# Performance work log

Hardware: AMD Instinct MI355X
Metric: run time of the kernel (lower is better)

The kernel has to match this reference:

```python
import jax, jax.numpy as jnp
import numpy as np

B, L, D = 16, 1024, 256
H, FF = 8, 2048
DH = D // H
EPS = 1e-5


def setup_inputs() -> dict:
    key = jax.random.key(0)
    ks = jax.random.split(key, 13)
    s = 0.02
    return {
        "x": jax.random.normal(ks[0], (B, L, D), jnp.float32),
        "Wq": jax.random.normal(ks[1], (D, D), jnp.float32) * s,
        "bq": jnp.zeros((D,), jnp.float32),
        "Wk": jax.random.normal(ks[2], (D, D), jnp.float32) * s,
        "bk": jnp.zeros((D,), jnp.float32),
        "Wv": jax.random.normal(ks[3], (D, D), jnp.float32) * s,
        "bv": jnp.zeros((D,), jnp.float32),
        "Wo": jax.random.normal(ks[4], (D, D), jnp.float32) * s,
        "bo": jnp.zeros((D,), jnp.float32),
        "W1": jax.random.normal(ks[5], (D, FF), jnp.float32) * s,
        "b1": jnp.zeros((FF,), jnp.float32),
        "W2": jax.random.normal(ks[6], (FF, D), jnp.float32) * s,
        "b2": jnp.zeros((D,), jnp.float32),
        "g1": jnp.ones((D,), jnp.float32),
        "be1": jnp.zeros((D,), jnp.float32),
        "g2": jnp.ones((D,), jnp.float32),
        "be2": jnp.zeros((D,), jnp.float32),
    }


def _layernorm(x, g, b):
    m = jnp.mean(x, axis=-1, keepdims=True)
    v = jnp.mean(jnp.square(x - m), axis=-1, keepdims=True)
    return (x - m) * jax.lax.rsqrt(v + EPS) * g + b


def reference(x, Wq, bq, Wk, bk, Wv, bv, Wo, bo, W1, b1, W2, b2, g1, be1, g2, be2):
    b, l, d = x.shape
    # QKV projections, split heads (torch split/cat == reshape to [b,l,H,dh])
    q = (x @ Wq + bq).reshape(b, l, H, DH)
    k = (x @ Wk + bk).reshape(b, l, H, DH)
    v = (x @ Wv + bv).reshape(b, l, H, DH)
    # scaled dot-product attention per head
    scores = jnp.einsum("bqhd,bkhd->bhqk", q, k) / np.float32(DH) ** 0.5
    attn = jax.nn.softmax(scores, axis=-1)
    o = jnp.einsum("bhqk,bkhd->bqhd", attn, v).reshape(b, l, d)
    o = o @ Wo + bo
    # residual + LN1 (dropout p=0.0 -> identity)
    h = _layernorm(x + o, g1, be1)
    # FFN + residual + LN2
    ff = jax.nn.relu(h @ W1 + b1) @ W2 + b2
    return _layernorm(h + ff, g2, be2)
```

## Files before the change

kernel.cpp:

```cpp
#include <hip/hip_runtime.h>
#include <math.h>

#define B_  16
#define L_  1024
#define D_  256
#define H_  8
#define DH_ 32
#define FF_ 2048
#define NROW (B_*L_)
#define QKVS 768

typedef __attribute__((ext_vector_type(8))) short short8;
typedef __attribute__((ext_vector_type(4))) short short4v;
typedef __attribute__((ext_vector_type(4))) float f32x4;
typedef __attribute__((ext_vector_type(4))) unsigned uint4v;
typedef unsigned short ushortT;

__device__ inline ushortT f2bf(float f) {
    unsigned u = __builtin_bit_cast(unsigned, f);
    u += 0x7fffu + ((u >> 16) & 1u);
    return (ushortT)(u >> 16);
}

__device__ inline float bf2f(ushortT u) {
    return __builtin_bit_cast(float, (unsigned)u << 16);
}

__device__ inline float fexp2(float x) {
#if __has_builtin(__builtin_amdgcn_exp2f)
    return __builtin_amdgcn_exp2f(x);
#else
    return exp2f(x);
#endif
}

__device__ inline void gload_lds16(const ushortT* g, ushortT* l) {
    __builtin_amdgcn_global_load_lds(
        (const __attribute__((address_space(1))) unsigned*)g,
        (__attribute__((address_space(3))) unsigned*)l, 16, 0, 0);
}

__device__ inline unsigned lds_addr(const void* p) {
    return (unsigned)(size_t)(const __attribute__((address_space(3))) void*)p;
}

template<bool RELU, bool OBF16>
__global__ __launch_bounds__(256)
void gemm_bf16_kernel(const ushortT* __restrict__ A, const ushortT* __restrict__ Bt,
                      const float* __restrict__ bias, void* __restrict__ Cv,
                      int M, int N, int K, int ldb, int ldc)
{
    __shared__ ushortT As[2][128 * 32];
    __shared__ ushortT Bs[2][128 * 32];

    const int tid   = threadIdx.x;
    const int w     = tid >> 6;
    const int lane  = tid & 63;
    const int qlane = lane & 15;
    const int g     = lane >> 4;
    const int wm    = w >> 1, wn = w & 1;
    const int m0    = blockIdx.y * 128;
    const int n0    = blockIdx.x * 128;

    int srowA[2], sq[2];
    #pragma unroll
    for (int j = 0; j < 2; ++j) {
        int idx = (j * 4 + w) * 64 + lane;
        srowA[j] = idx >> 2;
        sq[j]    = idx & 3;
    }

    f32x4 acc[4][4];
    #pragma unroll
    for (int mi = 0; mi < 4; ++mi)
        #pragma unroll
        for (int ni = 0; ni < 4; ++ni)
            acc[mi][ni] = (f32x4){0.f, 0.f, 0.f, 0.f};

    auto stage = [&](int buf, int kt) {
        const int k0 = kt * 32;
        #pragma unroll
        for (int j = 0; j < 2; ++j) {
            gload_lds16(A + (size_t)(m0 + srowA[j]) * K + k0 + sq[j] * 8,
                        &As[buf][(j * 4 + w) * 512]);
            gload_lds16(Bt + (size_t)(n0 + srowA[j]) * ldb + k0 + sq[j] * 8,
                        &Bs[buf][(j * 4 + w) * 512]);
        }
    };

    stage(0, 0);
    __syncthreads();

    const int nt = K >> 5;
    for (int t = 0; t < nt; ++t) {
        const int cur = t & 1;
        if (t + 1 < nt) stage(cur ^ 1, t + 1);

        short8 af[4], bfr[4];
        #pragma unroll
        for (int mi = 0; mi < 4; ++mi)
            af[mi] = *(const short8*)&As[cur][(wm * 64 + mi * 16 + qlane) * 32 + g * 8];
        #pragma unroll
        for (int ni = 0; ni < 4; ++ni)
            bfr[ni] = *(const short8*)&Bs[cur][(wn * 64 + ni * 16 + qlane) * 32 + g * 8];

        #pragma unroll
        for (int mi = 0; mi < 4; ++mi)
            #pragma unroll
            for (int ni = 0; ni < 4; ++ni)
                acc[mi][ni] = __builtin_amdgcn_mfma_f32_16x16x32_bf16(
                    af[mi], bfr[ni], acc[mi][ni], 0, 0, 0);

        __syncthreads();
    }

    #pragma unroll
    for (int mi = 0; mi < 4; ++mi) {
        #pragma unroll
        for (int ni = 0; ni < 4; ++ni) {
            const int n = n0 + wn * 64 + ni * 16 + qlane;
            const float bval = bias ? bias[n] : 0.f;
            #pragma unroll
            for (int r = 0; r < 4; ++r) {
                const int m = m0 + wm * 64 + mi * 16 + 4 * g + r;
                float v = acc[mi][ni][r] + bval;
                if (RELU)  v = fmaxf(v, 0.f);
                if (OBF16) ((ushortT*)Cv)[(size_t)m * ldc + n] = f2bf(v);
                else       ((float*)Cv)[(size_t)m * ldc + n] = v;
            }
        }
    }
}

template<bool RESF32, bool OBF16>
__global__ __launch_bounds__(512)
void gemm_ln_kernel(const ushortT* __restrict__ A, const ushortT* __restrict__ Bt,
                    const float* __restrict__ bias, const void* __restrict__ resid,
                    const float* __restrict__ gamma, const float* __restrict__ beta,
                    void* __restrict__ out, int K)
{
    __shared__ ushortT As[2][64 * 32];
    __shared__ ushortT Bs[2][256 * 32];
    __shared__ float part[8][32][2];
    __shared__ float rstat[64][2];

    const int tid   = threadIdx.x;
    const int w     = tid >> 6;
    const int lane  = tid & 63;
    const int qlane = lane & 15;
    const int g     = lane >> 4;
    const int wm    = w >> 2, wn = w & 3;
    const int m0    = blockIdx.x * 64;

    f32x4 acc[2][4];
    #pragma unroll
    for (int mi = 0; mi < 2; ++mi)
        #pragma unroll
        for (int ni = 0; ni < 4; ++ni)
            acc[mi][ni] = (f32x4){0.f, 0.f, 0.f, 0.f};

    const int r4 = lane >> 2, q8 = (lane & 3) * 8;

    auto stage = [&](int buf, int kt) {
        const int k0 = kt * 32;
        if (w < 4)
            gload_lds16(A + (size_t)(m0 + w * 16 + r4) * K + k0 + q8,
                        &As[buf][w * 512]);
        #pragma unroll
        for (int j = 0; j < 2; ++j) {
            const int c = w * 2 + j;
            gload_lds16(Bt + (size_t)(c * 16 + r4) * K + k0 + q8,
                        &Bs[buf][c * 512]);
        }
    };

    stage(0, 0);
    __syncthreads();

    const int nt = K >> 5;
    for (int t = 0; t < nt; ++t) {
        const int cur = t & 1;
        if (t + 1 < nt) stage(cur ^ 1, t + 1);

        short8 af[2], bfr[4];
        #pragma unroll
        for (int mi = 0; mi < 2; ++mi)
            af[mi] = *(const short8*)&As[cur][(wm * 32 + mi * 16 + qlane) * 32 + g * 8];
        #pragma unroll
        for (int ni = 0; ni < 4; ++ni)
            bfr[ni] = *(const short8*)&Bs[cur][(wn * 64 + ni * 16 + qlane) * 32 + g * 8];

        #pragma unroll
        for (int mi = 0; mi < 2; ++mi)
            #pragma unroll
            for (int ni = 0; ni < 4; ++ni)
                acc[mi][ni] = __builtin_amdgcn_mfma_f32_16x16x32_bf16(
                    af[mi], bfr[ni], acc[mi][ni], 0, 0, 0);

        __syncthreads();
    }

    #pragma unroll
    for (int ni = 0; ni < 4; ++ni) {
        const int n = wn * 64 + ni * 16 + qlane;
        const float bv = bias[n];
        #pragma unroll
        for (int mi = 0; mi < 2; ++mi)
            #pragma unroll
            for (int r = 0; r < 4; ++r) {
                const size_t m = (size_t)(m0 + wm * 32 + mi * 16 + 4 * g + r);
                float rv;
                if (RESF32) rv = ((const float*)resid)[m * 256 + n];
                else        rv = bf2f(((const ushortT*)resid)[m * 256 + n]);
                acc[mi][ni][r] += bv + rv;
            }
    }

    #pragma unroll
    for (int mi = 0; mi < 2; ++mi)
        #pragma unroll
        for (int r = 0; r < 4; ++r) {
            float s = 0.f, sq = 0.f;
            #pragma unroll
            for (int ni = 0; ni < 4; ++ni) {
                float hv = acc[mi][ni][r];
                s += hv; sq += hv * hv;
            }
            #pragma unroll
            for (int off = 1; off < 16; off <<= 1) {
                s  += __shfl_xor(s, off);
                sq += __shfl_xor(sq, off);
            }
            if (qlane == 0) {
                part[w][mi * 16 + 4 * g + r][0] = s;
                part[w][mi * 16 + 4 * g + r][1] = sq;
            }
        }
    __syncthreads();
    if (tid < 64) {
        const int wmr = tid >> 5, lrow = tid & 31;
        float s = 0.f, sq = 0.f;
        #pragma unroll
        for (int j = 0; j < 4; ++j) {
            s  += part[wmr * 4 + j][lrow][0];
            sq += part[wmr * 4 + j][lrow][1];
        }
        const float mean = s * (1.f / 256.f);
        const float var  = sq * (1.f / 256.f) - mean * mean;
        rstat[tid][0] = mean;
        rstat[tid][1] = rsqrtf(var + 1e-5f);
    }
    __syncthreads();

    float gam[4], bet[4];
    #pragma unroll
    for (int ni = 0; ni < 4; ++ni) {
        gam[ni] = gamma[wn * 64 + ni * 16 + qlane];
        bet[ni] = beta [wn * 64 + ni * 16 + qlane];
    }
    #pragma unroll
    for (int mi = 0; mi < 2; ++mi)
        #pragma unroll
        for (int r = 0; r < 4; ++r) {
            const int rloc = wm * 32 + mi * 16 + 4 * g + r;
            const float mean = rstat[rloc][0], rinv = rstat[rloc][1];
            const size_t m = (size_t)(m0 + rloc);
            #pragma unroll
            for (int ni = 0; ni < 4; ++ni) {
                const int n = wn * 64 + ni * 16 + qlane;
                const float val = (acc[mi][ni][r] - mean) * rinv * gam[ni] + bet[ni];
                if (OBF16) ((ushortT*)out)[m * 256 + n] = f2bf(val);
                else       ((float*)out)[m * 256 + n] = val;
            }
        }
}

__global__ __launch_bounds__(256)
void attn_mfma_kernel(const ushortT* __restrict__ qkv, ushortT* __restrict__ o)
{
    __shared__ __align__(16) ushortT K4[2][2048];
    __shared__ __align__(16) ushortT Vs[2][2048];

    const int tid   = threadIdx.x;
    const int lane  = tid & 63;
    const int w     = tid >> 6;
    const int qlane = lane & 15;
    const int g     = lane >> 4;

    const int bid = blockIdx.x;
    const int bh  = bid & 127;
    const int b   = bh >> 3;
    const int h   = bh & 7;
    const int q0  = (bid >> 7) * 64;

    const size_t inbase = (size_t)b * L_ * QKVS + h * 32;
    const size_t obase  = (size_t)b * L_ * 256 + h * 32;

    const short8 qf = *(const short8*)(qkv + inbase + (size_t)(q0 + w * 16 + qlane) * QKVS + g * 8);

    f32x4 ot0 = {0.f, 0.f, 0.f, 0.f}, ot1 = {0.f, 0.f, 0.f, 0.f};
    float l_reg = 0.f;

    const float CEXP = 0.25503540f;

    const int skey = tid >> 2;
    const int sg   = tid & 3;
    const ushortT* ksrc = qkv + inbase + 256 + sg * 8 + (size_t)skey * QKVS;
    const ushortT* vsrc = qkv + inbase + 512 + sg * 8 + (size_t)skey * QKVS;

    char* K4b = (char*)&K4[0][0];
    char* Vsb = (char*)&Vs[0][0];

    const unsigned vwoff = ((unsigned)((skey >> 2) * 2 + (sg >> 1))) * 128u +
                           ((unsigned)(skey & 3)) * 32u +
                           ((((unsigned)(sg & 1)) ^ ((unsigned)(sg >> 1))) * 16u);
    unsigned kwoff = (unsigned)sg * 1024u + (unsigned)skey * 16u;
    kwoff ^= (kwoff >> 5) & 0x60;
    unsigned kroff[4];
    #pragma unroll
    for (int kt4 = 0; kt4 < 4; ++kt4) {
        unsigned off = (unsigned)g * 1024u + (unsigned)(kt4 * 16 + qlane) * 16u;
        kroff[kt4] = off ^ ((off >> 5) & 0x60);
    }
    const unsigned vrbase  = lds_addr(&Vs[0][0]) + 256u * (unsigned)g + 8u * (unsigned)qlane;
    const unsigned vrbase2 = vrbase ^ 64u;

    short8 kreg = *(const short8*)ksrc;
    short8 vreg = *(const short8*)vsrc;

    #pragma unroll 2
    for (int t = 0; t < L_ / 64; ++t) {
        const unsigned bo = (unsigned)(t & 1) * 4096u;
        *(short8*)(K4b + bo + kwoff) = kreg;
        *(short8*)(Vsb + bo + vwoff) = vreg;
        if (t + 1 < L_ / 64) {
            const size_t roff = (size_t)((t + 1) * 64) * QKVS;
            kreg = *(const short8*)(ksrc + roff);
            vreg = *(const short8*)(vsrc + roff);
        }
        __syncthreads();

        f32x4 st[4];
        __builtin_amdgcn_s_setprio(1);
        #pragma unroll
        for (int kt4 = 0; kt4 < 4; ++kt4) {
            short8 kf = *(const short8*)(K4b + bo + kroff[kt4]);
            st[kt4] = __builtin_amdgcn_mfma_f32_16x16x32_bf16(kf, qf, (f32x4){0.f,0.f,0.f,0.f}, 0, 0, 0);
        }
        __builtin_amdgcn_s_setprio(0);

        float p[16];
        float s4[4];
        #pragma unroll
        for (int kt4 = 0; kt4 < 4; ++kt4) {
            #pragma unroll
            for (int r = 0; r < 4; ++r)
                p[kt4 * 4 + r] = fexp2(st[kt4][r] * CEXP);
            s4[kt4] = (p[kt4*4] + p[kt4*4+1]) + (p[kt4*4+2] + p[kt4*4+3]);
        }
        float ssum = (s4[0] + s4[1]) + (s4[2] + s4[3]);
        ssum += __shfl_xor(ssum, 16);
        ssum += __shfl_xor(ssum, 32);
        l_reg += ssum;

        unsigned pk_[8];
        #pragma unroll
        for (int i = 0; i < 8; ++i)
            asm("v_cvt_pk_bf16_f32 %0, %1, %2" : "=v"(pk_[i]) : "v"(p[2*i]), "v"(p[2*i+1]));
        const short8 pa0 = __builtin_bit_cast(short8, (uint4v){pk_[0], pk_[1], pk_[2], pk_[3]});
        const short8 pa1 = __builtin_bit_cast(short8, (uint4v){pk_[4], pk_[5], pk_[6], pk_[7]});

        const unsigned va  = vrbase  + bo;
        const unsigned va2 = vrbase2 + bo;
        __builtin_amdgcn_s_setprio(1);
        {
            short4v v00, v01, v10, v11;
            asm volatile("ds_read_b64_tr_b16 %0, %1"             : "=v"(v00) : "v"(va));
            asm volatile("ds_read_b64_tr_b16 %0, %1 offset:1024" : "=v"(v01) : "v"(va));
            asm volatile("ds_read_b64_tr_b16 %0, %1 offset:128"  : "=v"(v10) : "v"(va2));
            asm volatile("ds_read_b64_tr_b16 %0, %1 offset:1152" : "=v"(v11) : "v"(va2));
            asm volatile("s_waitcnt lgkmcnt(0)" ::: "memory");
            __builtin_amdgcn_sched_barrier(0);
            short8 vb0 = __builtin_shufflevector(v00, v01, 0,1,2,3,4,5,6,7);
            short8 vb1 = __builtin_shufflevector(v10, v11, 0,1,2,3,4,5,6,7);
            ot0 = __builtin_amdgcn_mfma_f32_16x16x32_bf16(pa0, vb0, ot0, 0, 0, 0);
            ot1 = __builtin_amdgcn_mfma_f32_16x16x32_bf16(pa0, vb1, ot1, 0, 0, 0);
        }
        {
            short4v v00, v01, v10, v11;
            asm volatile("ds_read_b64_tr_b16 %0, %1 offset:2048" : "=v"(v00) : "v"(va));
            asm volatile("ds_read_b64_tr_b16 %0, %1 offset:3072" : "=v"(v01) : "v"(va));
            asm volatile("ds_read_b64_tr_b16 %0, %1 offset:2176" : "=v"(v10) : "v"(va2));
            asm volatile("ds_read_b64_tr_b16 %0, %1 offset:3200" : "=v"(v11) : "v"(va2));
            asm volatile("s_waitcnt lgkmcnt(0)" ::: "memory");
            __builtin_amdgcn_sched_barrier(0);
            short8 vb0 = __builtin_shufflevector(v00, v01, 0,1,2,3,4,5,6,7);
            short8 vb1 = __builtin_shufflevector(v10, v11, 0,1,2,3,4,5,6,7);
            ot0 = __builtin_amdgcn_mfma_f32_16x16x32_bf16(pa1, vb0, ot0, 0, 0, 0);
            ot1 = __builtin_amdgcn_mfma_f32_16x16x32_bf16(pa1, vb1, ot1, 0, 0, 0);
        }
        __builtin_amdgcn_s_setprio(0);
    }

    const float linv = 1.f / l_reg;
    #pragma unroll
    for (int r = 0; r < 4; ++r) {
        float lr = __shfl(linv, 4 * g + r);
        size_t row = (size_t)(q0 + w * 16 + 4 * g + r);
        ushortT* op = o + obase + row * 256;
        op[qlane]      = f2bf(ot0[r] * lr);
        op[16 + qlane] = f2bf(ot1[r] * lr);
    }
}

__global__ __launch_bounds__(256)
void prep_kernel(const float* __restrict__ x, ushortT* __restrict__ xb,
                 const float* __restrict__ Wq, const float* __restrict__ Wk,
                 const float* __restrict__ Wv, const float* __restrict__ Wo,
                 ushortT* __restrict__ Wqkvb, ushortT* __restrict__ Wob,
                 const float* __restrict__ W1, ushortT* __restrict__ W1b,
                 const float* __restrict__ W2, ushortT* __restrict__ W2b,
                 const float* __restrict__ bq, const float* __restrict__ bk,
                 const float* __restrict__ bv, float* __restrict__ bqkv)
{
    __shared__ float t[32][33];
    const int bid = blockIdx.x;
    const int tid = threadIdx.x;

    if (bid < 4096) {
        const int i = (bid * 256 + tid) * 4;
        float4 v = *reinterpret_cast<const float4*>(x + i);
        unsigned p0 = (unsigned)f2bf(v.x) | ((unsigned)f2bf(v.y) << 16);
        unsigned p1 = (unsigned)f2bf(v.z) | ((unsigned)f2bf(v.w) << 16);
        uint2 u = {p0, p1};
        *reinterpret_cast<uint2*>(xb + i) = u;
        return;
    }
    int i = bid - 4096;
    const float* W; ushortT* Wt; int K, N, bx, by;
    if (i < 256) {
        const int which = i >> 6, j = i & 63;
        bx = j & 7; by = j >> 3; K = 256; N = 256;
        W  = which == 0 ? Wq : which == 1 ? Wk : which == 2 ? Wv : Wo;
        Wt = which == 0 ? Wqkvb : which == 1 ? Wqkvb + 65536
           : which == 2 ? Wqkvb + 131072 : Wob;
    } else if (i < 768) {
        const int j = i - 256; bx = j & 63; by = j >> 6; K = 256; N = 2048;
        W = W1; Wt = W1b;
    } else if (i < 1280) {
        const int j = i - 768; bx = j & 7; by = j >> 3; K = 2048; N = 256;
        W = W2; Wt = W2b;
    } else {
        for (int k = tid; k < 768; k += 256)
            bqkv[k] = k < 256 ? bq[k] : (k < 512 ? bk[k - 256] : bv[k - 512]);
        return;
    }
    const int tx = tid & 31, ty = tid >> 5;
    const int k0 = by * 32, n0 = bx * 32;
    #pragma unroll
    for (int r = ty; r < 32; r += 8) t[r][tx] = W[(size_t)(k0 + r) * N + n0 + tx];
    __syncthreads();
    #pragma unroll
    for (int r = ty; r < 32; r += 8) Wt[(size_t)(n0 + r) * K + k0 + tx] = f2bf(t[tx][r]);
}

extern "C" void kernel_launch(void* const* d_in, const int* in_sizes, int n_in,
                              void* d_out, int out_size, void* d_ws, size_t ws_size,
                              hipStream_t stream)
{
    const float* x   = (const float*)d_in[0];
    const float* Wq  = (const float*)d_in[1];
    const float* bq  = (const float*)d_in[2];
    const float* Wk  = (const float*)d_in[3];
    const float* bk  = (const float*)d_in[4];
    const float* Wv  = (const float*)d_in[5];
    const float* bv  = (const float*)d_in[6];
    const float* Wo  = (const float*)d_in[7];
    const float* bo  = (const float*)d_in[8];
    const float* W1  = (const float*)d_in[9];
    const float* b1  = (const float*)d_in[10];
    const float* W2  = (const float*)d_in[11];
    const float* b2  = (const float*)d_in[12];
    const float* g1  = (const float*)d_in[13];
    const float* be1 = (const float*)d_in[14];
    const float* g2  = (const float*)d_in[15];
    const float* be2 = (const float*)d_in[16];
    float* out = (float*)d_out;

    char* wsb = (char*)d_ws;
    const size_t MB = (size_t)1 << 20;
    ushortT* Wqkvb = (ushortT*)(wsb);
    ushortT* Wob   = (ushortT*)(wsb + 393216);
    ushortT* W1b   = (ushortT*)(wsb + 1 * MB);
    ushortT* W2b   = (ushortT*)(wsb + 2 * MB);
    float*   bqkv  = (float*)  (wsb + 3 * MB);
    ushortT* xb  = (ushortT*)(wsb + 4 * MB);
    ushortT* qkv = (ushortT*)(wsb + 12 * MB);
    ushortT* ob  = (ushortT*)(wsb + 36 * MB);
    ushortT* hb  = (ushortT*)(wsb + 4 * MB);
    ushortT* f1  = (ushortT*)(wsb + 12 * MB);

    prep_kernel<<<dim3(5377), dim3(256), 0, stream>>>(
        x, xb, Wq, Wk, Wv, Wo, Wqkvb, Wob, W1, W1b, W2, W2b, bq, bk, bv, bqkv);

    gemm_bf16_kernel<false, true><<<dim3(6, 128), dim3(256), 0, stream>>>(
        xb, Wqkvb, bqkv, qkv, NROW, QKVS, 256, 256, QKVS);

    attn_mfma_kernel<<<dim3(2048), dim3(256), 0, stream>>>(qkv, ob);

    gemm_ln_kernel<true, true><<<dim3(256), dim3(512), 0, stream>>>(
        ob, Wob, bo, x, g1, be1, hb, 256);

    gemm_bf16_kernel<true, true><<<dim3(16, 128), dim3(256), 0, stream>>>(
        hb, W1b, b1, f1, NROW, FF_, 256, 256, FF_);

    gemm_ln_kernel<false, false><<<dim3(256), dim3(512), 0, stream>>>(
        f1, W2b, b2, hb, g2, be2, out, 2048);
}
```

Before: 153.8 us.

## Shrink GEMM+LayerNorm row tile to 32 rows and launch 512 blocks

The fused GEMM+LayerNorm kernel now handles 32 rows per block instead of 64. Each of the 8 waves owns a 32-column slice across all rows, and the grid doubles to 512 blocks. The aim is better occupancy across the CUs: 256 blocks is roughly one per CU on MI355X, so doubling the count should fill the device and hide load latency. In exchange, each block reloads the full 256-column B tile for half as many rows, doubling weight traffic per output row and lowering MFMA reuse per LDS load.

```diff
diff --git a/kernel.cpp b/kernel.cpp
--- a/kernel.cpp
+++ b/kernel.cpp
@@ -139,38 +139,35 @@
                     const float* __restrict__ gamma, const float* __restrict__ beta,
                     void* __restrict__ out, int K)
 {
-    __shared__ ushortT As[2][64 * 32];
+    __shared__ ushortT As[2][32 * 32];
     __shared__ ushortT Bs[2][256 * 32];
     __shared__ float part[8][32][2];
-    __shared__ float rstat[64][2];
+    __shared__ float rstat[32][2];
 
     const int tid   = threadIdx.x;
     const int w     = tid >> 6;
     const int lane  = tid & 63;
     const int qlane = lane & 15;
     const int g     = lane >> 4;
-    const int wm    = w >> 2, wn = w & 3;
-    const int m0    = blockIdx.x * 64;
-
-    f32x4 acc[2][4];
+    const int m0    = blockIdx.x * 32;
+
+    f32x4 acc[2][2];
     #pragma unroll
     for (int mi = 0; mi < 2; ++mi)
         #pragma unroll
-        for (int ni = 0; ni < 4; ++ni)
+        for (int ni = 0; ni < 2; ++ni)
             acc[mi][ni] = (f32x4){0.f, 0.f, 0.f, 0.f};
-
-    const int r4 = lane >> 2, q8 = (lane & 3) * 8;
 
     auto stage = [&](int buf, int kt) {
         const int k0 = kt * 32;
-        if (w < 4)
-            gload_lds16(A + (size_t)(m0 + w * 16 + r4) * K + k0 + q8,
-                        &As[buf][w * 512]);
+        if (tid < 128)
+            gload_lds16(A + (size_t)(m0 + (tid >> 2)) * K + k0 + (tid & 3) * 8,
+                        &As[buf][tid * 8]);
         #pragma unroll
         for (int j = 0; j < 2; ++j) {
-            const int c = w * 2 + j;
-            gload_lds16(Bt + (size_t)(c * 16 + r4) * K + k0 + q8,
-                        &Bs[buf][c * 512]);
+            const int idx = j * 512 + tid;
+            gload_lds16(Bt + (size_t)(idx >> 2) * K + k0 + (idx & 3) * 8,
+                        &Bs[buf][idx * 8]);
         }
     };
 
@@ -182,18 +179,18 @@
         const int cur = t & 1;
         if (t + 1 < nt) stage(cur ^ 1, t + 1);
 
-        short8 af[2], bfr[4];
+        short8 af[2], bfr[2];
         #pragma unroll
         for (int mi = 0; mi < 2; ++mi)
-            af[mi] = *(const short8*)&As[cur][(wm * 32 + mi * 16 + qlane) * 32 + g * 8];
-        #pragma unroll
-        for (int ni = 0; ni < 4; ++ni)
-            bfr[ni] = *(const short8*)&Bs[cur][(wn * 64 + ni * 16 + qlane) * 32 + g * 8];
+            af[mi] = *(const short8*)&As[cur][(mi * 16 + qlane) * 32 + g * 8];
+        #pragma unroll
+        for (int ni = 0; ni < 2; ++ni)
+            bfr[ni] = *(const short8*)&Bs[cur][(w * 32 + ni * 16 + qlane) * 32 + g * 8];
 
         #pragma unroll
         for (int mi = 0; mi < 2; ++mi)
             #pragma unroll
-            for (int ni = 0; ni < 4; ++ni)
+            for (int ni = 0; ni < 2; ++ni)
                 acc[mi][ni] = __builtin_amdgcn_mfma_f32_16x16x32_bf16(
                     af[mi], bfr[ni], acc[mi][ni], 0, 0, 0);
 
@@ -201,14 +198,14 @@
     }
 
     #pragma unroll
-    for (int ni = 0; ni < 4; ++ni) {
-        const int n = wn * 64 + ni * 16 + qlane;
+    for (int ni = 0; ni < 2; ++ni) {
+        const int n = w * 32 + ni * 16 + qlane;
         const float bv = bias[n];
         #pragma unroll
         for (int mi = 0; mi < 2; ++mi)
             #pragma unroll
             for (int r = 0; r < 4; ++r) {
-                const size_t m = (size_t)(m0 + wm * 32 + mi * 16 + 4 * g + r);
+                const size_t m = (size_t)(m0 + mi * 16 + 4 * g + r);
                 float rv;
                 if (RESF32) rv = ((const float*)resid)[m * 256 + n];
                 else        rv = bf2f(((const ushortT*)resid)[m * 256 + n]);
@@ -222,7 +219,7 @@
         for (int r = 0; r < 4; ++r) {
             float s = 0.f, sq = 0.f;
             #pragma unroll
-            for (int ni = 0; ni < 4; ++ni) {
+            for (int ni = 0; ni < 2; ++ni) {
                 float hv = acc[mi][ni][r];
                 s += hv; sq += hv * hv;
             }
@@ -237,13 +234,12 @@
             }
         }
     __syncthreads();
-    if (tid < 64) {
-        const int wmr = tid >> 5, lrow = tid & 31;
+    if (tid < 32) {
         float s = 0.f, sq = 0.f;
         #pragma unroll
-        for (int j = 0; j < 4; ++j) {
-            s  += part[wmr * 4 + j][lrow][0];
-            sq += part[wmr * 4 + j][lrow][1];
+        for (int j = 0; j < 8; ++j) {
+            s  += part[j][tid][0];
+            sq += part[j][tid][1];
         }
         const float mean = s * (1.f / 256.f);
         const float var  = sq * (1.f / 256.f) - mean * mean;
@@ -252,22 +248,22 @@
     }
     __syncthreads();
 
-    float gam[4], bet[4];
-    #pragma unroll
-    for (int ni = 0; ni < 4; ++ni) {
-        gam[ni] = gamma[wn * 64 + ni * 16 + qlane];
-        bet[ni] = beta [wn * 64 + ni * 16 + qlane];
+    float gam[2], bet[2];
+    #pragma unroll
+    for (int ni = 0; ni < 2; ++ni) {
+        gam[ni] = gamma[w * 32 + ni * 16 + qlane];
+        bet[ni] = beta [w * 32 + ni * 16 + qlane];
     }
     #pragma unroll
     for (int mi = 0; mi < 2; ++mi)
         #pragma unroll
         for (int r = 0; r < 4; ++r) {
-            const int rloc = wm * 32 + mi * 16 + 4 * g + r;
+            const int rloc = mi * 16 + 4 * g + r;
             const float mean = rstat[rloc][0], rinv = rstat[rloc][1];
             const size_t m = (size_t)(m0 + rloc);
             #pragma unroll
-            for (int ni = 0; ni < 4; ++ni) {
-                const int n = wn * 64 + ni * 16 + qlane;
+            for (int ni = 0; ni < 2; ++ni) {
+                const int n = w * 32 + ni * 16 + qlane;
                 const float val = (acc[mi][ni][r] - mean) * rinv * gam[ni] + bet[ni];
                 if (OBF16) ((ushortT*)out)[m * 256 + n] = f2bf(val);
                 else       ((float*)out)[m * 256 + n] = val;
@@ -508,12 +504,12 @@
 
     attn_mfma_kernel<<<dim3(2048), dim3(256), 0, stream>>>(qkv, ob);
 
-    gemm_ln_kernel<true, true><<<dim3(256), dim3(512), 0, stream>>>(
+    gemm_ln_kernel<true, true><<<dim3(512), dim3(512), 0, stream>>>(
         ob, Wob, bo, x, g1, be1, hb, 256);
 
     gemm_bf16_kernel<true, true><<<dim3(16, 128), dim3(256), 0, stream>>>(
         hb, W1b, b1, f1, NROW, FF_, 256, 256, FF_);
 
-    gemm_ln_kernel<false, false><<<dim3(256), dim3(512), 0, stream>>>(
+    gemm_ln_kernel<false, false><<<dim3(512), dim3(512), 0, stream>>>(
         f1, W2b, b2, hb, g2, be2, out, 2048);
 }
```

Result: no change. 155.0 us (+0.8%).

## Split fused GEMM+LayerNorm into 64x64-tile GEMM and separate LayerNorm kernel

Applied to the files above, without the earlier changes.

Replaces the fused GEMM+residual+LayerNorm kernel, whose 64-row by full-256-column tiles gave only 256 blocks, with a 64x64-tile GEMM launching 1024 blocks plus a standalone row-wise LayerNorm kernel that adds the residual. The aim is more parallelism and occupancy for the Wo and W2 projections. In exchange the projection output goes through global memory an extra time, one more launch is added per LayerNorm, and the W2 GEMM now writes fp32 output that the LayerNorm then rewrites in place. The workspace offsets are also repacked so the new intermediate buffer fits.

```diff
diff --git a/kernel.cpp b/kernel.cpp
--- a/kernel.cpp
+++ b/kernel.cpp
@@ -14,6 +14,7 @@
 typedef __attribute__((ext_vector_type(4))) short short4v;
 typedef __attribute__((ext_vector_type(4))) float f32x4;
 typedef __attribute__((ext_vector_type(4))) unsigned uint4v;
+typedef __attribute__((ext_vector_type(4))) unsigned short ushort4v;
 typedef unsigned short ushortT;
 
 __device__ inline ushortT f2bf(float f) {
@@ -132,46 +133,33 @@
     }
 }
 
-template<bool RESF32, bool OBF16>
-__global__ __launch_bounds__(512)
-void gemm_ln_kernel(const ushortT* __restrict__ A, const ushortT* __restrict__ Bt,
-                    const float* __restrict__ bias, const void* __restrict__ resid,
-                    const float* __restrict__ gamma, const float* __restrict__ beta,
-                    void* __restrict__ out, int K)
+template<bool OBF16>
+__global__ __launch_bounds__(256)
+void gemm64_kernel(const ushortT* __restrict__ A, const ushortT* __restrict__ Bt,
+                   const float* __restrict__ bias, void* __restrict__ Cv, int K)
 {
     __shared__ ushortT As[2][64 * 32];
-    __shared__ ushortT Bs[2][256 * 32];
-    __shared__ float part[8][32][2];
-    __shared__ float rstat[64][2];
+    __shared__ ushortT Bs[2][64 * 32];
 
     const int tid   = threadIdx.x;
     const int w     = tid >> 6;
     const int lane  = tid & 63;
     const int qlane = lane & 15;
     const int g     = lane >> 4;
-    const int wm    = w >> 2, wn = w & 3;
-    const int m0    = blockIdx.x * 64;
-
-    f32x4 acc[2][4];
-    #pragma unroll
-    for (int mi = 0; mi < 2; ++mi)
-        #pragma unroll
-        for (int ni = 0; ni < 4; ++ni)
-            acc[mi][ni] = (f32x4){0.f, 0.f, 0.f, 0.f};
-
-    const int r4 = lane >> 2, q8 = (lane & 3) * 8;
+    const int m0    = blockIdx.y * 64;
+    const int n0    = blockIdx.x * 64;
+
+    const int srow = tid >> 2;
+    const int sq   = tid & 3;
+
+    f32x4 acc[4];
+    #pragma unroll
+    for (int ni = 0; ni < 4; ++ni) acc[ni] = (f32x4){0.f, 0.f, 0.f, 0.f};
 
     auto stage = [&](int buf, int kt) {
         const int k0 = kt * 32;
-        if (w < 4)
-            gload_lds16(A + (size_t)(m0 + w * 16 + r4) * K + k0 + q8,
-                        &As[buf][w * 512]);
-        #pragma unroll
-        for (int j = 0; j < 2; ++j) {
-            const int c = w * 2 + j;
-            gload_lds16(Bt + (size_t)(c * 16 + r4) * K + k0 + q8,
-                        &Bs[buf][c * 512]);
-        }
+        gload_lds16(A + (size_t)(m0 + srow) * K + k0 + sq * 8, &As[buf][w * 512]);
+        gload_lds16(Bt + (size_t)(n0 + srow) * K + k0 + sq * 8, &Bs[buf][w * 512]);
     };
 
     stage(0, 0);
@@ -182,97 +170,92 @@
         const int cur = t & 1;
         if (t + 1 < nt) stage(cur ^ 1, t + 1);
 
-        short8 af[2], bfr[4];
-        #pragma unroll
-        for (int mi = 0; mi < 2; ++mi)
-            af[mi] = *(const short8*)&As[cur][(wm * 32 + mi * 16 + qlane) * 32 + g * 8];
+        short8 af = *(const short8*)&As[cur][(w * 16 + qlane) * 32 + g * 8];
+        short8 bfr[4];
         #pragma unroll
         for (int ni = 0; ni < 4; ++ni)
-            bfr[ni] = *(const short8*)&Bs[cur][(wn * 64 + ni * 16 + qlane) * 32 + g * 8];
-
-        #pragma unroll
-        for (int mi = 0; mi < 2; ++mi)
-            #pragma unroll
-            for (int ni = 0; ni < 4; ++ni)
-                acc[mi][ni] = __builtin_amdgcn_mfma_f32_16x16x32_bf16(
-                    af[mi], bfr[ni], acc[mi][ni], 0, 0, 0);
+            bfr[ni] = *(const short8*)&Bs[cur][(ni * 16 + qlane) * 32 + g * 8];
+
+        #pragma unroll
+        for (int ni = 0; ni < 4; ++ni)
+            acc[ni] = __builtin_amdgcn_mfma_f32_16x16x32_bf16(af, bfr[ni], acc[ni], 0, 0, 0);
 
         __syncthreads();
     }
 
     #pragma unroll
     for (int ni = 0; ni < 4; ++ni) {
-        const int n = wn * 64 + ni * 16 + qlane;
-        const float bv = bias[n];
-        #pragma unroll
-        for (int mi = 0; mi < 2; ++mi)
-            #pragma unroll
-            for (int r = 0; r < 4; ++r) {
-                const size_t m = (size_t)(m0 + wm * 32 + mi * 16 + 4 * g + r);
-                float rv;
-                if (RESF32) rv = ((const float*)resid)[m * 256 + n];
-                else        rv = bf2f(((const ushortT*)resid)[m * 256 + n]);
-                acc[mi][ni][r] += bv + rv;
-            }
-    }
-
-    #pragma unroll
-    for (int mi = 0; mi < 2; ++mi)
+        const int n = n0 + ni * 16 + qlane;
+        const float bval = bias[n];
         #pragma unroll
         for (int r = 0; r < 4; ++r) {
-            float s = 0.f, sq = 0.f;
-            #pragma unroll
-            for (int ni = 0; ni < 4; ++ni) {
-                float hv = acc[mi][ni][r];
-                s += hv; sq += hv * hv;
-            }
-            #pragma unroll
-            for (int off = 1; off < 16; off <<= 1) {
-                s  += __shfl_xor(s, off);
-                sq += __shfl_xor(sq, off);
-            }
-            if (qlane == 0) {
-                part[w][mi * 16 + 4 * g + r][0] = s;
-                part[w][mi * 16 + 4 * g + r][1] = sq;
-            }
-        }
-    __syncthreads();
-    if (tid < 64) {
-        const int wmr = tid >> 5, lrow = tid & 31;
-        float s = 0.f, sq = 0.f;
-        #pragma unroll
-        for (int j = 0; j < 4; ++j) {
-            s  += part[wmr * 4 + j][lrow][0];
-            sq += part[wmr * 4 + j][lrow][1];
-        }
-        const float mean = s * (1.f / 256.f);
-        const float var  = sq * (1.f / 256.f) - mean * mean;
-        rstat[tid][0] = mean;
-        rstat[tid][1] = rsqrtf(var + 1e-5f);
-    }
-    __syncthreads();
-
-    float gam[4], bet[4];
-    #pragma unroll
-    for (int ni = 0; ni < 4; ++ni) {
-        gam[ni] = gamma[wn * 64 + ni * 16 + qlane];
-        bet[ni] = beta [wn * 64 + ni * 16 + qlane];
-    }
-    #pragma unroll
-    for (int mi = 0; mi < 2; ++mi)
-        #pragma unroll
-        for (int r = 0; r < 4; ++r) {
-            const int rloc = wm * 32 + mi * 16 + 4 * g + r;
-            const float mean = rstat[rloc][0], rinv = rstat[rloc][1];
-            const size_t m = (size_t)(m0 + rloc);
-            #pragma unroll
-            for (int ni = 0; ni < 4; ++ni) {
-                const int n = wn * 64 + ni * 16 + qlane;
-                const float val = (acc[mi][ni][r] - mean) * rinv * gam[ni] + bet[ni];
-                if (OBF16) ((ushortT*)out)[m * 256 + n] = f2bf(val);
-                else       ((float*)out)[m * 256 + n] = val;
-            }
-        }
+            const int m = m0 + w * 16 + 4 * g + r;
+            float v = acc[ni][r] + bval;
+            if (OBF16) ((ushortT*)Cv)[(size_t)m * D_ + n] = f2bf(v);
+            else       ((float*)Cv)[(size_t)m * D_ + n] = v;
+        }
+    }
+}
+
+template<bool XF32, bool YF32, bool OBF16>
+__global__ __launch_bounds__(256)
+void ln_kernel(const void* __restrict__ X, const void* __restrict__ Y,
+               const float* __restrict__ g, const float* __restrict__ bb,
+               void* __restrict__ out)
+{
+    const int tid  = threadIdx.x;
+    const int lane = tid & 63;
+    const int w    = tid >> 6;
+    const size_t row = (size_t)blockIdx.x * 4 + w;
+    const int c    = lane * 4;
+
+    float xv[4], yv[4];
+    if (XF32) {
+        float4 v = *reinterpret_cast<const float4*>((const float*)X + row * D_ + c);
+        xv[0] = v.x; xv[1] = v.y; xv[2] = v.z; xv[3] = v.w;
+    } else {
+        ushort4v v = *reinterpret_cast<const ushort4v*>((const ushortT*)X + row * D_ + c);
+        #pragma unroll
+        for (int j = 0; j < 4; ++j) xv[j] = bf2f(v[j]);
+    }
+    if (YF32) {
+        float4 v = *reinterpret_cast<const float4*>((const float*)Y + row * D_ + c);
+        yv[0] = v.x; yv[1] = v.y; yv[2] = v.z; yv[3] = v.w;
+    } else {
+        ushort4v v = *reinterpret_cast<const ushort4v*>((const ushortT*)Y + row * D_ + c);
+        #pragma unroll
+        for (int j = 0; j < 4; ++j) yv[j] = bf2f(v[j]);
+    }
+
+    float s0 = xv[0] + yv[0], s1 = xv[1] + yv[1], s2 = xv[2] + yv[2], s3 = xv[3] + yv[3];
+
+    float sum = s0 + s1 + s2 + s3;
+    float sq  = s0 * s0 + s1 * s1 + s2 * s2 + s3 * s3;
+    #pragma unroll
+    for (int off = 1; off < 64; off <<= 1) {
+        sum += __shfl_xor(sum, off);
+        sq  += __shfl_xor(sq, off);
+    }
+    const float mean = sum * (1.f / D_);
+    const float var  = sq * (1.f / D_) - mean * mean;
+    const float rinv = rsqrtf(var + 1e-5f);
+
+    const float4 gv = *reinterpret_cast<const float4*>(g + c);
+    const float4 bv = *reinterpret_cast<const float4*>(bb + c);
+    float o0 = (s0 - mean) * rinv * gv.x + bv.x;
+    float o1 = (s1 - mean) * rinv * gv.y + bv.y;
+    float o2 = (s2 - mean) * rinv * gv.z + bv.z;
+    float o3 = (s3 - mean) * rinv * gv.w + bv.w;
+
+    if (OBF16) {
+        unsigned p0 = (unsigned)f2bf(o0) | ((unsigned)f2bf(o1) << 16);
+        unsigned p1 = (unsigned)f2bf(o2) | ((unsigned)f2bf(o3) << 16);
+        uint2 u = {p0, p1};
+        *reinterpret_cast<uint2*>((ushortT*)out + row * D_ + c) = u;
+    } else {
+        float4 ov = {o0, o1, o2, o3};
+        *reinterpret_cast<float4*>((float*)out + row * D_ + c) = ov;
+    }
 }
 
 __global__ __launch_bounds__(256)
@@ -491,14 +474,15 @@
     const size_t MB = (size_t)1 << 20;
     ushortT* Wqkvb = (ushortT*)(wsb);
     ushortT* Wob   = (ushortT*)(wsb + 393216);
-    ushortT* W1b   = (ushortT*)(wsb + 1 * MB);
-    ushortT* W2b   = (ushortT*)(wsb + 2 * MB);
-    float*   bqkv  = (float*)  (wsb + 3 * MB);
-    ushortT* xb  = (ushortT*)(wsb + 4 * MB);
-    ushortT* qkv = (ushortT*)(wsb + 12 * MB);
-    ushortT* ob  = (ushortT*)(wsb + 36 * MB);
-    ushortT* hb  = (ushortT*)(wsb + 4 * MB);
-    ushortT* f1  = (ushortT*)(wsb + 12 * MB);
+    ushortT* W1b   = (ushortT*)(wsb + 512 * 1024);
+    ushortT* W2b   = (ushortT*)(wsb + 1536 * 1024);
+    float*   bqkv  = (float*)  (wsb + 2560 * 1024);
+    ushortT* xb  = (ushortT*)(wsb + 3 * MB);
+    ushortT* qkv = (ushortT*)(wsb + 11 * MB);
+    ushortT* ob  = (ushortT*)(wsb + 35 * MB);
+    ushortT* ao  = (ushortT*)(wsb + 43 * MB);
+    ushortT* hb  = (ushortT*)(wsb + 3 * MB);
+    ushortT* f1  = (ushortT*)(wsb + 11 * MB);
 
     prep_kernel<<<dim3(5377), dim3(256), 0, stream>>>(
         x, xb, Wq, Wk, Wv, Wo, Wqkvb, Wob, W1, W1b, W2, W2b, bq, bk, bv, bqkv);
@@ -508,12 +492,16 @@
 
     attn_mfma_kernel<<<dim3(2048), dim3(256), 0, stream>>>(qkv, ob);
 
-    gemm_ln_kernel<true, true><<<dim3(256), dim3(512), 0, stream>>>(
-        ob, Wob, bo, x, g1, be1, hb, 256);
+    gemm64_kernel<true><<<dim3(4, 256), dim3(256), 0, stream>>>(ob, Wob, bo, ao, 256);
+
+    ln_kernel<true, false, true><<<dim3(NROW / 4), dim3(256), 0, stream>>>(
+        x, ao, g1, be1, hb);
 
     gemm_bf16_kernel<true, true><<<dim3(16, 128), dim3(256), 0, stream>>>(
         hb, W1b, b1, f1, NROW, FF_, 256, 256, FF_);
 
-    gemm_ln_kernel<false, false><<<dim3(256), dim3(512), 0, stream>>>(
-        f1, W2b, b2, hb, g2, be2, out, 2048);
-}
+    gemm64_kernel<false><<<dim3(4, 256), dim3(256), 0, stream>>>(f1, W2b, b2, out, 2048);
+
+    ln_kernel<false, true, false><<<dim3(NROW / 4), dim3(256), 0, stream>>>(
+        hb, out, g2, be2, out);
+}
```

Result: slower. 165.4 us (+7.6%).
